# Optimization experiments

Measured on AMD Instinct MI355X. Metric: run time of the kernel, lower is better.

The kernel has to match this reference:

```python
import jax, jax.numpy as jnp
import numpy as np

MAX_SEGMENTS = 256
MAX_PIXELS = 400   # fixed-capacity bucket per segment
EMBED_DIM = 768
N_CHANNELS = 3


def setup_inputs() -> dict:
    key = jax.random.key(0)
    k1, k2, k3, k4 = jax.random.split(key, 4)
    img = jax.random.normal(k1, (32, N_CHANNELS, 384, 384), dtype=jnp.float32)
    segments = jax.random.randint(k2, (32, 384, 384), 0, MAX_SEGMENTS, dtype=jnp.int32)
    fan_in = N_CHANNELS * MAX_PIXELS
    proj_w = jax.random.normal(k3, (EMBED_DIM, fan_in), dtype=jnp.float32) / np.sqrt(fan_in).astype(np.float32)
    proj_b = jax.random.normal(k4, (EMBED_DIM,), dtype=jnp.float32) * 0.01
    return {"img": img, "segments": segments, "proj_w": proj_w, "proj_b": proj_b}


def _bucketize(img_flat, seg_flat):
    """img_flat: [C, N] pixels in row-major scan order; seg_flat: [N] int ids.
    Returns [S, C*P]: first P pixels (scan order) of each segment, zero padded,
    channel-major per segment — matching torch's masked gather + flatten."""
    C, N = img_flat.shape
    idx = jnp.arange(N, dtype=jnp.int32)
    # stable sort by segment id preserves scan order within each segment
    order = jnp.argsort(seg_flat, stable=True)
    sorted_seg = seg_flat[order]
    is_start = jnp.concatenate([jnp.ones((1,), bool), sorted_seg[1:] != sorted_seg[:-1]])
    group_start = jax.lax.cummax(jnp.where(is_start, idx, 0))
    rank_sorted = idx - group_start                      # position within segment
    rank = jnp.zeros((N,), jnp.int32).at[order].set(rank_sorted)
    dump = MAX_SEGMENTS * MAX_PIXELS                      # overflow slot (discarded)
    dest = jnp.where(rank < MAX_PIXELS, seg_flat.astype(jnp.int32) * MAX_PIXELS + rank, dump)
    buf = jnp.zeros((C, dump + 1), img_flat.dtype).at[:, dest].set(img_flat)
    # [C, S, P] -> [S, C, P] -> [S, C*P] (channel-major flatten per segment)
    return buf[:, :dump].reshape(C, MAX_SEGMENTS, MAX_PIXELS).transpose(1, 0, 2).reshape(MAX_SEGMENTS, C * MAX_PIXELS)


def reference(img, segments, proj_w, proj_b):
    B, C, H, W = img.shape
    feats = jax.vmap(_bucketize)(img.reshape(B, C, H * W), segments.reshape(B, H * W))
    # [B, S, C*P] @ [C*P, E] + [E]
    return feats @ proj_w.T + proj_b
```

## Files before the change

### kernel.cpp

```cpp
#include <hip/hip_runtime.h>
#include <hip/hip_bf16.h>
#include <cstdint>

#define BATCH 32
#define NCH 3
#define HW 147456
#define NSEG 256
#define NPIX 400
#define KDIM 1200
#define EDIM 768
#define MROWS (BATCH * NSEG)

#define CHUNK 4096
#define NCHUNK (HW / CHUNK)
#define NW 16
#define SUBW (CHUNK / NW)

#define ROW_BYTES 4800
#define APK_BYTES ((size_t)MROWS * ROW_BYTES)
#define W_BYTES (EDIM * KDIM * 4)

typedef __attribute__((ext_vector_type(8))) short short8b;
typedef __attribute__((ext_vector_type(16))) float f32x16;

__device__ __forceinline__ uint32_t bf16_rn(float f) {
    uint32_t u = __float_as_uint(f);
    return (u + 0x7fffu + ((u >> 16) & 1u)) >> 16;
}
__device__ __forceinline__ float bf16_tof(uint32_t h) { return __uint_as_float(h << 16); }
__device__ __forceinline__ uint32_t pack_split(float v) {
    uint32_t hi = bf16_rn(v);
    uint32_t lo = bf16_rn(v - bf16_tof(hi));
    return (lo << 16) | hi;
}

__device__ __forceinline__ void async_copy16(const void* gsrc, void* ldst) {
    __builtin_amdgcn_global_load_lds(
        (const __attribute__((address_space(1))) uint32_t*)gsrc,
        (__attribute__((address_space(3))) uint32_t*)ldst, 16, 0, 0);
}

__global__ __launch_bounds__(256) void hist_kernel(const int* __restrict__ seg,
                                                   int* __restrict__ cnt) {
    __shared__ int h[NSEG];
    const int tid = threadIdx.x;
    h[tid] = 0;
    __syncthreads();
    const int blk = blockIdx.x;
    const int b = blk / NCHUNK, ck = blk % NCHUNK;
    const int* segb = seg + (size_t)b * HW + ck * CHUNK;
#pragma unroll
    for (int i = 0; i < CHUNK / 256; ++i) atomicAdd(&h[segb[i * 256 + tid]], 1);
    __syncthreads();
    cnt[blk * NSEG + tid] = h[tid];
}

__global__ __launch_bounds__(256) void scan_kernel(int* __restrict__ cnt) {
    const int t = blockIdx.x * 256 + threadIdx.x;
    const int b = t >> 8, s = t & 255;
    int* basep = cnt + (size_t)(b * NCHUNK) * NSEG + s;
    int v[NCHUNK];
#pragma unroll
    for (int ck = 0; ck < NCHUNK; ++ck) v[ck] = basep[ck * NSEG];
    int run = 0;
#pragma unroll
    for (int ck = 0; ck < NCHUNK; ++ck) { const int x = v[ck]; v[ck] = run; run += x; }
    v[0] = run;
#pragma unroll
    for (int ck = 0; ck < NCHUNK; ++ck) basep[ck * NSEG] = v[ck];
}

__global__ __launch_bounds__(1024) void scatter_kernel(const float* __restrict__ img,
                                                       const int* __restrict__ seg,
                                                       const int* __restrict__ base,
                                                       uint8_t* __restrict__ apk) {
    __shared__ int wpos[NW][NSEG];
    __shared__ int sbv[NSEG];
    __shared__ int sl[NSEG];
    __shared__ uint8_t segmap[CHUNK];
    __shared__ uint32_t st0[CHUNK], st1[CHUNK], st2[CHUNK];

    const int tid = threadIdx.x;
    const int lane = tid & 63;
    const int wid = tid >> 6;
    const int blk = blockIdx.x;
    const int b = blk / NCHUNK, ck = blk % NCHUNK;

    if (tid < NSEG) sbv[tid] = (ck == 0) ? 0 : base[(size_t)blk * NSEG + tid];
#pragma unroll
    for (int i = 0; i < (NW * NSEG) / 1024; ++i) ((int*)wpos)[i * 1024 + tid] = 0;
    __syncthreads();

    const int* segb = seg + (size_t)b * HW;
    const float* imgb = img + (size_t)b * NCH * HW;
    const int startp = ck * CHUNK + wid * SUBW;
    const unsigned long long lt = (lane == 0) ? 0ull : ((~0ull) >> (64 - lane));

    int sv[SUBW / 64];
    unsigned long long mv[SUBW / 64];
#pragma unroll
    for (int g = 0; g < SUBW / 64; ++g) {
        const int p = startp + g * 64 + lane;
        const int s = segb[p];
        unsigned long long m = ~0ull;
#pragma unroll
        for (int bit = 0; bit < 8; ++bit) {
            unsigned long long bal = __ballot((s >> bit) & 1);
            m &= ((s >> bit) & 1) ? bal : ~bal;
        }
        sv[g] = s; mv[g] = m;
        if ((m & lt) == 0ull) atomicAdd(&wpos[wid][s], __popcll(m));
    }
    __syncthreads();

    if (tid < NSEG) {
        int r = sbv[tid];
#pragma unroll
        for (int w = 0; w < NW; ++w) {
            const int t = wpos[w][tid];
            wpos[w][tid] = r;
            r += t;
        }
        sl[tid] = r - sbv[tid];
    }
    __syncthreads();

    if (wid == 0) {
        int v0 = sl[lane * 4], v1 = sl[lane * 4 + 1], v2 = sl[lane * 4 + 2], v3 = sl[lane * 4 + 3];
        const int mysum = v0 + v1 + v2 + v3;
        int run = mysum;
#pragma unroll
        for (int off = 1; off < 64; off <<= 1) {
            const int y = __shfl_up(run, off, 64);
            if (lane >= off) run += y;
        }
        int e = run - mysum;
        sl[lane * 4]     = (sbv[lane * 4]     << 13) | e;  e += v0;
        sl[lane * 4 + 1] = (sbv[lane * 4 + 1] << 13) | e;  e += v1;
        sl[lane * 4 + 2] = (sbv[lane * 4 + 2] << 13) | e;  e += v2;
        sl[lane * 4 + 3] = (sbv[lane * 4 + 3] << 13) | e;
    }
    __syncthreads();

#pragma unroll
    for (int g = 0; g < SUBW / 64; ++g) {
        const int p = startp + g * 64 + lane;
        const int s = sv[g];
        const unsigned long long m = mv[g];
        const int rig = __popcll(m & lt);
        const int leader = __ffsll((unsigned long long)m) - 1;
        int old = 0;
        if (rig == 0) old = atomicAdd(&wpos[wid][s], __popcll(m));
        old = __shfl(old, leader, 64);
        const int rank = old + rig;
        const int v = sl[s];
        const int j = rank - (v >> 13) + (v & 8191);
        st0[j] = pack_split(imgb[p]);
        st1[j] = pack_split(imgb[HW + p]);
        st2[j] = pack_split(imgb[2 * HW + p]);
        segmap[j] = (uint8_t)s;
    }
    __syncthreads();

    uint8_t* apkb = apk + (size_t)b * NSEG * ROW_BYTES;
#pragma unroll
    for (int it = 0; it < CHUNK / 1024; ++it) {
        const int j = it * 1024 + tid;
        const int s = segmap[j];
        const int v = sl[s];
        const int rank = (v >> 13) + (j - (v & 8191));
        if (rank < NPIX) {
            uint16_t* hp = (uint16_t*)(apkb + (size_t)s * ROW_BYTES);
            uint16_t* lp = (uint16_t*)(apkb + (size_t)s * ROW_BYTES + 2400);
            const uint32_t v0 = st0[j], v1 = st1[j], v2 = st2[j];
            hp[rank]       = (uint16_t)v0;  lp[rank]       = (uint16_t)(v0 >> 16);
            hp[400 + rank] = (uint16_t)v1;  lp[400 + rank] = (uint16_t)(v1 >> 16);
            hp[800 + rank] = (uint16_t)v2;  lp[800 + rank] = (uint16_t)(v2 >> 16);
        }
    }
}

__global__ __launch_bounds__(256) void tailzero_kernel(uint8_t* __restrict__ apk,
                                                       const int* __restrict__ cnt) {
    const int tid = threadIdx.x;
    const int l = tid & 63;
    const int wid = tid >> 6;
    const int row = blockIdx.x * 4 + wid;
    const int b = row >> 8, s = row & 255;
    const int tot = cnt[(size_t)(b * NCHUNK) * NSEG + s];
    if (tot >= NPIX) return;
    uint16_t* hp = (uint16_t*)(apk + (size_t)row * ROW_BYTES);
    uint16_t* lp = (uint16_t*)(apk + (size_t)row * ROW_BYTES + 2400);
    for (int r = tot + l; r < NPIX; r += 64) {
        hp[r] = 0; lp[r] = 0;
        hp[400 + r] = 0; lp[400 + r] = 0;
        hp[800 + r] = 0; lp[800 + r] = 0;
    }
}

__global__ __launch_bounds__(256) void repackW_kernel(float* __restrict__ w) {
    __shared__ float buf[4][KDIM];
    const int tid = threadIdx.x;
    const int l = tid & 63;
    const int wid = tid >> 6;
    const int row = blockIdx.x * 4 + wid;
    float* rowp = w + (size_t)row * KDIM;
#pragma unroll
    for (int i = 0; i < 19; ++i) {
        const int idx = i * 64 + l;
        if (idx < KDIM) buf[wid][idx] = rowp[idx];
    }
    __syncthreads();
    uint32_t* rowu = (uint32_t*)rowp;
#pragma unroll
    for (int i = 0; i < 10; ++i) {
        const int j = i * 64 + l;
        if (j < KDIM / 2) {
            const float f0 = buf[wid][2 * j], f1 = buf[wid][2 * j + 1];
            const uint32_t h0 = bf16_rn(f0), h1 = bf16_rn(f1);
            const uint32_t l0 = bf16_rn(f0 - bf16_tof(h0));
            const uint32_t l1 = bf16_rn(f1 - bf16_tof(h1));
            rowu[j]            = h0 | (h1 << 16);
            rowu[KDIM / 2 + j] = l0 | (l1 << 16);
        }
    }
}

__global__ __launch_bounds__(256) void gemm_kernel(const uint8_t* __restrict__ A,
                                                   const uint8_t* __restrict__ Wp,
                                                   const float* __restrict__ bias,
                                                   float* __restrict__ out) {
    __shared__ uint8_t smem[49152];

    const int tid = threadIdx.x;
    const int l = tid & 63;
    const int wid = tid >> 6;
    const int wm = wid >> 1, wn = wid & 1;

    const int bid = blockIdx.x;
    const int xcd = bid & 7;
    const int t = bid >> 3;
    const int bn = t % 12;
    const int bm = (t / 12) * 8 + xcd;

    const int swzl = ((l & 7) * 16) ^ ((l >> 3) << 4);
    const int xread = (l & 7) << 4;

    const uint8_t* Abase = A + (size_t)bm * 128 * ROW_BYTES;

    f32x16 acc[2] = {};

    for (int k0 = 0; k0 < KDIM; k0 += 64) {
#pragma unroll
        for (int ii = 0; ii < 4; ++ii) {
            const int i = wid * 4 + ii;
            const int row = i * 8 + (l >> 3);
            const size_t gb = (size_t)row * ROW_BYTES + k0 * 2 + swzl;
            async_copy16(Abase + gb,        smem + i * 1024);
            async_copy16(Abase + gb + 2400, smem + 16384 + i * 1024);
        }
#pragma unroll
        for (int ii = 0; ii < 2; ++ii) {
            const int i = wid * 2 + ii;
            const int row = i * 8 + (l >> 3);
            const size_t gb = (size_t)(bn * 64 + row) * ROW_BYTES + k0 * 2 + swzl;
            async_copy16(Wp + gb, smem + 32768 + i * 1024);
            size_t gl = gb + 2400;
            if (gl + 16 > (size_t)W_BYTES) gl = 0;
            async_copy16(Wp + gl, smem + 40960 + i * 1024);
        }
        __syncthreads();

#pragma unroll
        for (int ks = 0; ks < 4; ++ks) {
            if (k0 + ks * 16 >= KDIM) break;
            const int koff = ks * 32 + ((l >> 5) * 16);
            short8b ahi[2], alo[2], bhi, blo;
#pragma unroll
            for (int mi = 0; mi < 2; ++mi) {
                const int row = wm * 64 + mi * 32 + (l & 31);
                const int byteA = row * 128 + (koff ^ xread);
                ahi[mi] = *(const short8b*)(smem + byteA);
                alo[mi] = *(const short8b*)(smem + 16384 + byteA);
            }
            {
                const int row = wn * 32 + (l & 31);
                const int byteB = row * 128 + (koff ^ xread);
                bhi = *(const short8b*)(smem + 32768 + byteB);
                blo = *(const short8b*)(smem + 40960 + byteB);
            }
#pragma unroll
            for (int mi = 0; mi < 2; ++mi) {
                acc[mi] = __builtin_amdgcn_mfma_f32_32x32x16_bf16(ahi[mi], bhi, acc[mi], 0, 0, 0);
                acc[mi] = __builtin_amdgcn_mfma_f32_32x32x16_bf16(ahi[mi], blo, acc[mi], 0, 0, 0);
                acc[mi] = __builtin_amdgcn_mfma_f32_32x32x16_bf16(alo[mi], bhi, acc[mi], 0, 0, 0);
            }
        }
        __syncthreads();
    }

    const int e = bn * 64 + wn * 32 + (l & 31);
    const float bv = bias[e];
#pragma unroll
    for (int mi = 0; mi < 2; ++mi) {
        const int rbase = bm * 128 + wm * 64 + mi * 32 + 4 * (l >> 5);
#pragma unroll
        for (int r = 0; r < 16; ++r) {
            const int row = rbase + (r & 3) + 8 * (r >> 2);
            out[(size_t)row * EDIM + e] = acc[mi][r] + bv;
        }
    }
}

extern "C" void kernel_launch(void* const* d_in, const int* in_sizes, int n_in,
                              void* d_out, int out_size, void* d_ws, size_t ws_size,
                              hipStream_t stream) {
    const float* img      = (const float*)d_in[0];
    const int*   segments = (const int*)d_in[1];
    float*       proj_w   = (float*)d_in[2];
    const float* proj_b   = (const float*)d_in[3];
    float* out = (float*)d_out;

    uint8_t* apk = (uint8_t*)d_ws;
    int*     cnt = (int*)((char*)d_ws + APK_BYTES);

    hist_kernel<<<BATCH * NCHUNK, 256, 0, stream>>>(segments, cnt);
    scan_kernel<<<MROWS / 256, 256, 0, stream>>>(cnt);
    repackW_kernel<<<EDIM / 4, 256, 0, stream>>>(proj_w);
    scatter_kernel<<<BATCH * NCHUNK, 1024, 0, stream>>>(img, segments, cnt, apk);
    tailzero_kernel<<<MROWS / 4, 256, 0, stream>>>(apk, cnt);

    gemm_kernel<<<64 * 12, 256, 0, stream>>>(apk, (const uint8_t*)proj_w, proj_b, out);
}
```

Before: 212.4 us.

## Fuse prep kernels and double-buffer GEMM K-loop with async LDS loads

Merges the histogram and the W bf16 split-repack into one launch, with per-wave sub-histograms to cut LDS atomic contention. Tail zeroing moves into the last scatter chunk block, which removes two kernel launches. The GEMM now uses a 32-wide K step with two LDS buffers: the next tile is prefetched while the current one runs through MFMA, guarded by vmcnt waits and raw barriers. The new LDS swizzle and the single-thread serial tail zero loop add correctness risk. The tail zero loop may also be slow for segments with few pixels.

```diff
diff --git a/kernel.cpp b/kernel.cpp
--- a/kernel.cpp
+++ b/kernel.cpp
@@ -15,6 +15,7 @@
 #define NCHUNK (HW / CHUNK)
 #define NW 16
 #define SUBW (CHUNK / NW)
+#define HIST_BLOCKS (BATCH * NCHUNK)
 
 #define ROW_BYTES 4800
 #define APK_BYTES ((size_t)MROWS * ROW_BYTES)
@@ -40,19 +41,51 @@
         (__attribute__((address_space(3))) uint32_t*)ldst, 16, 0, 0);
 }
 
-__global__ __launch_bounds__(256) void hist_kernel(const int* __restrict__ seg,
-                                                   int* __restrict__ cnt) {
-    __shared__ int h[NSEG];
+__global__ __launch_bounds__(256) void histW_kernel(const int* __restrict__ seg,
+                                                    int* __restrict__ cnt,
+                                                    float* __restrict__ w) {
+    __shared__ uint32_t sbuf[4 * KDIM];
     const int tid = threadIdx.x;
-    h[tid] = 0;
-    __syncthreads();
-    const int blk = blockIdx.x;
-    const int b = blk / NCHUNK, ck = blk % NCHUNK;
-    const int* segb = seg + (size_t)b * HW + ck * CHUNK;
-#pragma unroll
-    for (int i = 0; i < CHUNK / 256; ++i) atomicAdd(&h[segb[i * 256 + tid]], 1);
-    __syncthreads();
-    cnt[blk * NSEG + tid] = h[tid];
+    const int l = tid & 63;
+    const int wid = tid >> 6;
+
+    if (blockIdx.x < HIST_BLOCKS) {
+        int* h = (int*)sbuf;
+#pragma unroll
+        for (int i = 0; i < 4; ++i) h[i * NSEG + tid] = 0;
+        __syncthreads();
+        const int blk = blockIdx.x;
+        const int b = blk / NCHUNK, ck = blk % NCHUNK;
+        const int* segb = seg + (size_t)b * HW + ck * CHUNK;
+#pragma unroll
+        for (int i = 0; i < CHUNK / 256; ++i)
+            atomicAdd(&h[wid * NSEG + segb[i * 256 + tid]], 1);
+        __syncthreads();
+        cnt[blk * NSEG + tid] = h[tid] + h[NSEG + tid] + h[2 * NSEG + tid] + h[3 * NSEG + tid];
+    } else {
+        float* buf = (float*)sbuf;
+        const int row = (blockIdx.x - HIST_BLOCKS) * 4 + wid;
+        float* rowp = w + (size_t)row * KDIM;
+#pragma unroll
+        for (int i = 0; i < 19; ++i) {
+            const int idx = i * 64 + l;
+            if (idx < KDIM) buf[wid * KDIM + idx] = rowp[idx];
+        }
+        __syncthreads();
+        uint32_t* rowu = (uint32_t*)rowp;
+#pragma unroll
+        for (int i = 0; i < 10; ++i) {
+            const int j = i * 64 + l;
+            if (j < KDIM / 2) {
+                const float f0 = buf[wid * KDIM + 2 * j], f1 = buf[wid * KDIM + 2 * j + 1];
+                const uint32_t h0 = bf16_rn(f0), h1 = bf16_rn(f1);
+                const uint32_t l0 = bf16_rn(f0 - bf16_tof(h0));
+                const uint32_t l1 = bf16_rn(f1 - bf16_tof(h1));
+                rowu[j]            = h0 | (h1 << 16);
+                rowu[KDIM / 2 + j] = l0 | (l1 << 16);
+            }
+        }
+    }
 }
 
 __global__ __launch_bounds__(256) void scan_kernel(int* __restrict__ cnt) {
@@ -178,59 +211,29 @@
             hp[800 + rank] = (uint16_t)v2;  lp[800 + rank] = (uint16_t)(v2 >> 16);
         }
     }
-}
-
-__global__ __launch_bounds__(256) void tailzero_kernel(uint8_t* __restrict__ apk,
-                                                       const int* __restrict__ cnt) {
-    const int tid = threadIdx.x;
-    const int l = tid & 63;
-    const int wid = tid >> 6;
-    const int row = blockIdx.x * 4 + wid;
-    const int b = row >> 8, s = row & 255;
-    const int tot = cnt[(size_t)(b * NCHUNK) * NSEG + s];
-    if (tot >= NPIX) return;
-    uint16_t* hp = (uint16_t*)(apk + (size_t)row * ROW_BYTES);
-    uint16_t* lp = (uint16_t*)(apk + (size_t)row * ROW_BYTES + 2400);
-    for (int r = tot + l; r < NPIX; r += 64) {
-        hp[r] = 0; lp[r] = 0;
-        hp[400 + r] = 0; lp[400 + r] = 0;
-        hp[800 + r] = 0; lp[800 + r] = 0;
-    }
-}
-
-__global__ __launch_bounds__(256) void repackW_kernel(float* __restrict__ w) {
-    __shared__ float buf[4][KDIM];
-    const int tid = threadIdx.x;
-    const int l = tid & 63;
-    const int wid = tid >> 6;
-    const int row = blockIdx.x * 4 + wid;
-    float* rowp = w + (size_t)row * KDIM;
-#pragma unroll
-    for (int i = 0; i < 19; ++i) {
-        const int idx = i * 64 + l;
-        if (idx < KDIM) buf[wid][idx] = rowp[idx];
-    }
-    __syncthreads();
-    uint32_t* rowu = (uint32_t*)rowp;
-#pragma unroll
-    for (int i = 0; i < 10; ++i) {
-        const int j = i * 64 + l;
-        if (j < KDIM / 2) {
-            const float f0 = buf[wid][2 * j], f1 = buf[wid][2 * j + 1];
-            const uint32_t h0 = bf16_rn(f0), h1 = bf16_rn(f1);
-            const uint32_t l0 = bf16_rn(f0 - bf16_tof(h0));
-            const uint32_t l1 = bf16_rn(f1 - bf16_tof(h1));
-            rowu[j]            = h0 | (h1 << 16);
-            rowu[KDIM / 2 + j] = l0 | (l1 << 16);
-        }
-    }
-}
+
+    if (ck == NCHUNK - 1 && tid < NSEG) {
+        const int tot = base[(size_t)(b * NCHUNK) * NSEG + tid];
+        if (tot < NPIX) {
+            uint16_t* hp = (uint16_t*)(apkb + (size_t)tid * ROW_BYTES);
+            uint16_t* lp = (uint16_t*)(apkb + (size_t)tid * ROW_BYTES + 2400);
+            for (int r = tot; r < NPIX; ++r) {
+                hp[r] = 0; lp[r] = 0;
+                hp[400 + r] = 0; lp[400 + r] = 0;
+                hp[800 + r] = 0; lp[800 + r] = 0;
+            }
+        }
+    }
+}
+
+#define NT 38
+#define BUF_BYTES 24576
 
 __global__ __launch_bounds__(256) void gemm_kernel(const uint8_t* __restrict__ A,
                                                    const uint8_t* __restrict__ Wp,
                                                    const float* __restrict__ bias,
                                                    float* __restrict__ out) {
-    __shared__ uint8_t smem[49152];
+    __shared__ uint8_t smem[2 * BUF_BYTES];
 
     const int tid = threadIdx.x;
     const int l = tid & 63;
@@ -239,65 +242,83 @@
 
     const int bid = blockIdx.x;
     const int xcd = bid & 7;
-    const int t = bid >> 3;
-    const int bn = t % 12;
-    const int bm = (t / 12) * 8 + xcd;
-
-    const int swzl = ((l & 7) * 16) ^ ((l >> 3) << 4);
-    const int xread = (l & 7) << 4;
+    const int tq = bid >> 3;
+    const int bn = tq % 12;
+    const int bm = (tq / 12) * 8 + xcd;
+
+    const int csrc = ((l & 3) ^ ((l >> 3) & 3)) * 16;
+    const int rl4 = l >> 2;
+    const int lr31 = l & 31;
+    const int kcb = l >> 5;
+    const int fA = (lr31 >> 1) & 3;
 
     const uint8_t* Abase = A + (size_t)bm * 128 * ROW_BYTES;
+    const uint8_t* Bbase = Wp + (size_t)bn * 64 * ROW_BYTES;
 
     f32x16 acc[2] = {};
 
-    for (int k0 = 0; k0 < KDIM; k0 += 64) {
-#pragma unroll
-        for (int ii = 0; ii < 4; ++ii) {
-            const int i = wid * 4 + ii;
-            const int row = i * 8 + (l >> 3);
-            const size_t gb = (size_t)row * ROW_BYTES + k0 * 2 + swzl;
-            async_copy16(Abase + gb,        smem + i * 1024);
-            async_copy16(Abase + gb + 2400, smem + 16384 + i * 1024);
-        }
-#pragma unroll
-        for (int ii = 0; ii < 2; ++ii) {
-            const int i = wid * 2 + ii;
-            const int row = i * 8 + (l >> 3);
-            const size_t gb = (size_t)(bn * 64 + row) * ROW_BYTES + k0 * 2 + swzl;
-            async_copy16(Wp + gb, smem + 32768 + i * 1024);
-            size_t gl = gb + 2400;
-            if (gl + 16 > (size_t)W_BYTES) gl = 0;
-            async_copy16(Wp + gl, smem + 40960 + i * 1024);
-        }
-        __syncthreads();
-
-#pragma unroll
-        for (int ks = 0; ks < 4; ++ks) {
-            if (k0 + ks * 16 >= KDIM) break;
-            const int koff = ks * 32 + ((l >> 5) * 16);
-            short8b ahi[2], alo[2], bhi, blo;
-#pragma unroll
-            for (int mi = 0; mi < 2; ++mi) {
-                const int row = wm * 64 + mi * 32 + (l & 31);
-                const int byteA = row * 128 + (koff ^ xread);
-                ahi[mi] = *(const short8b*)(smem + byteA);
-                alo[mi] = *(const short8b*)(smem + 16384 + byteA);
+#define STAGE(t_, q_)                                                                   \
+    {                                                                                   \
+        const int k2 = (t_) * 64;                                                       \
+        uint8_t* bufb = smem + (q_) * BUF_BYTES;                                        \
+        _Pragma("unroll")                                                               \
+        for (int ii = 0; ii < 2; ++ii) {                                                \
+            const int i = wid * 2 + ii;                                                 \
+            const size_t gb = (size_t)(i * 16 + rl4) * ROW_BYTES + k2 + csrc;           \
+            async_copy16(Abase + gb,        bufb + i * 1024);                           \
+            async_copy16(Abase + gb + 2400, bufb + 8192 + i * 1024);                    \
+        }                                                                               \
+        {                                                                               \
+            const int row = wid * 16 + rl4;                                             \
+            const size_t gb = (size_t)row * ROW_BYTES + k2 + csrc;                      \
+            async_copy16(Bbase + gb, bufb + 16384 + wid * 1024);                        \
+            size_t gl = (size_t)(bn * 64 + row) * ROW_BYTES + k2 + csrc + 2400;         \
+            if (gl + 16 > (size_t)W_BYTES) gl = 0;     \
+            async_copy16(Wp + gl, bufb + 20480 + wid * 1024);                           \
+        }                                                                               \
+    }
+
+    STAGE(0, 0)
+    for (int t = 0; t < NT; ++t) {
+        if (t + 1 < NT) {
+            STAGE(t + 1, (t + 1) & 1)
+            asm volatile("s_waitcnt vmcnt(6)" ::: "memory");
+        } else {
+            asm volatile("s_waitcnt vmcnt(0)" ::: "memory");
+        }
+        __builtin_amdgcn_sched_barrier(0);
+        __builtin_amdgcn_s_barrier();
+
+        {
+            uint8_t* bufb = smem + (t & 1) * BUF_BYTES;
+            const int k0 = t * 32;
+#pragma unroll
+            for (int ks = 0; ks < 2; ++ks) {
+                if (k0 + ks * 16 >= KDIM) break;
+                const int cc = 16 * ((2 * ks + kcb) ^ fA);
+                short8b ahi[2], alo[2], bhi, blo;
+#pragma unroll
+                for (int mi = 0; mi < 2; ++mi) {
+                    const int ro = (wm * 64 + mi * 32 + lr31) * 64;
+                    ahi[mi] = *(const short8b*)(bufb + ro + cc);
+                    alo[mi] = *(const short8b*)(bufb + 8192 + ro + cc);
+                }
+                {
+                    const int ro = (wn * 32 + lr31) * 64;
+                    bhi = *(const short8b*)(bufb + 16384 + ro + cc);
+                    blo = *(const short8b*)(bufb + 20480 + ro + cc);
+                }
+#pragma unroll
+                for (int mi = 0; mi < 2; ++mi) {
+                    acc[mi] = __builtin_amdgcn_mfma_f32_32x32x16_bf16(ahi[mi], bhi, acc[mi], 0, 0, 0);
+                    acc[mi] = __builtin_amdgcn_mfma_f32_32x32x16_bf16(ahi[mi], blo, acc[mi], 0, 0, 0);
+                    acc[mi] = __builtin_amdgcn_mfma_f32_32x32x16_bf16(alo[mi], bhi, acc[mi], 0, 0, 0);
+                }
             }
-            {
-                const int row = wn * 32 + (l & 31);
-                const int byteB = row * 128 + (koff ^ xread);
-                bhi = *(const short8b*)(smem + 32768 + byteB);
-                blo = *(const short8b*)(smem + 40960 + byteB);
-            }
-#pragma unroll
-            for (int mi = 0; mi < 2; ++mi) {
-                acc[mi] = __builtin_amdgcn_mfma_f32_32x32x16_bf16(ahi[mi], bhi, acc[mi], 0, 0, 0);
-                acc[mi] = __builtin_amdgcn_mfma_f32_32x32x16_bf16(ahi[mi], blo, acc[mi], 0, 0, 0);
-                acc[mi] = __builtin_amdgcn_mfma_f32_32x32x16_bf16(alo[mi], bhi, acc[mi], 0, 0, 0);
-            }
-        }
-        __syncthreads();
-    }
+        }
+        __builtin_amdgcn_s_barrier();
+    }
+#undef STAGE
 
     const int e = bn * 64 + wn * 32 + (l & 31);
     const float bv = bias[e];
@@ -324,11 +345,9 @@
     uint8_t* apk = (uint8_t*)d_ws;
     int*     cnt = (int*)((char*)d_ws + APK_BYTES);
 
-    hist_kernel<<<BATCH * NCHUNK, 256, 0, stream>>>(segments, cnt);
+    histW_kernel<<<HIST_BLOCKS + EDIM / 4, 256, 0, stream>>>(segments, cnt, proj_w);
     scan_kernel<<<MROWS / 256, 256, 0, stream>>>(cnt);
-    repackW_kernel<<<EDIM / 4, 256, 0, stream>>>(proj_w);
     scatter_kernel<<<BATCH * NCHUNK, 1024, 0, stream>>>(img, segments, cnt, apk);
-    tailzero_kernel<<<MROWS / 4, 256, 0, stream>>>(apk, cnt);
 
     gemm_kernel<<<64 * 12, 256, 0, stream>>>(apk, (const uint8_t*)proj_w, proj_b, out);
 }
```

Measured after the change: 210.3 us. No clear change (-1.0%).
